# Kernel optimization log

Measured on AMD Instinct MI355X. Metric: run time of the kernel, lower is better.

Reference implementation:

```python
import jax, jax.numpy as jnp
import numpy as np

N_HEADS = 8
NEG_INF = -1e9


def setup_inputs() -> dict:
    key = jax.random.key(0)
    ks = jax.random.split(key, 9)
    B, S, D = 4, 2048, 512
    scale = 1.0 / np.sqrt(D)
    x = jax.random.normal(ks[0], (B, S, D), dtype=jnp.float32)
    mask = jnp.tril(jnp.ones((S, S), dtype=bool))[None, None, :, :]  # causal [1,1,S,S]
    W_Q_w = jax.random.normal(ks[1], (D, D), dtype=jnp.float32) * scale
    W_Q_b = jax.random.normal(ks[2], (D,), dtype=jnp.float32) * 0.02
    W_K_w = jax.random.normal(ks[3], (D, D), dtype=jnp.float32) * scale
    W_K_b = jax.random.normal(ks[4], (D,), dtype=jnp.float32) * 0.02
    W_V_w = jax.random.normal(ks[5], (D, D), dtype=jnp.float32) * scale
    W_V_b = jax.random.normal(ks[6], (D,), dtype=jnp.float32) * 0.02
    W_O_w = jax.random.normal(ks[7], (D, D), dtype=jnp.float32) * scale
    W_O_b = jax.random.normal(ks[8], (D,), dtype=jnp.float32) * 0.02
    return {"x": x, "mask": mask,
            "W_Q_w": W_Q_w, "W_Q_b": W_Q_b, "W_K_w": W_K_w, "W_K_b": W_K_b,
            "W_V_w": W_V_w, "W_V_b": W_V_b, "W_O_w": W_O_w, "W_O_b": W_O_b}


def reference(x, mask, W_Q_w, W_Q_b, W_K_w, W_K_b, W_V_w, W_V_b, W_O_w, W_O_b):
    B, S, D = x.shape
    H = N_HEADS
    Dh = D // H
    # projections (torch Linear: x @ W.T + b), split heads -> [B,H,S,Dh]
    def split_heads(t):
        return t.reshape(B, S, H, Dh).transpose(0, 2, 1, 3)
    Q = split_heads(x @ W_Q_w.T + W_Q_b)
    K = split_heads(x @ W_K_w.T + W_K_b)
    V = split_heads(x @ W_V_w.T + W_V_b)
    # scaled dot-product attention with explicit [B,H,S,S] scores
    scores = jnp.einsum("bhqd,bhkd->bhqk", Q, K) / jnp.sqrt(jnp.float32(Dh))
    scores = jnp.where(mask, scores, jnp.float32(NEG_INF))
    att = jax.nn.softmax(scores, axis=-1)
    out = jnp.einsum("bhqk,bhkd->bhqd", att, V)
    out = out.transpose(0, 2, 1, 3).reshape(B, S, D)
    return out @ W_O_w.T + W_O_b
```

## Files before the change

### kernel.cpp

```cpp
#include <hip/hip_runtime.h>
#include <hip/hip_bf16.h>

#define BATCH 4
#define SEQ   2048
#define DIM   512
#define NH    8
#define DH    64
#define NTOK  (BATCH*SEQ)

typedef __bf16 bf16x8 __attribute__((ext_vector_type(8)));
typedef float  f32x4  __attribute__((ext_vector_type(4)));

#define MFMA16(a,b,c) __builtin_amdgcn_mfma_f32_16x16x32_bf16((a),(b),(c),0,0,0)

#if __has_builtin(__builtin_amdgcn_exp2f)
#define EXP2F(x) __builtin_amdgcn_exp2f(x)
#else
#define EXP2F(x) exp2f(x)
#endif

#define QSCALE 0.18033688011112042f

typedef __attribute__((address_space(1))) void GAS;
typedef __attribute__((address_space(3))) void LAS;
__device__ __forceinline__ void gl_lds16(const void* g, void* l) {
  __builtin_amdgcn_global_load_lds((GAS*)g, (LAS*)l, 16, 0, 0);
}

__global__ __launch_bounds__(256) void cvt_f32_bf16(const float* __restrict__ src,
                                                    __bf16* __restrict__ dst, int n8) {
  int i = blockIdx.x * blockDim.x + threadIdx.x;
  if (i >= n8) return;
  const float4* s = (const float4*)src;
  float4 a = s[2*i], b = s[2*i+1];
  bf16x8 o;
  o[0] = (__bf16)a.x; o[1] = (__bf16)a.y; o[2] = (__bf16)a.z; o[3] = (__bf16)a.w;
  o[4] = (__bf16)b.x; o[5] = (__bf16)b.y; o[6] = (__bf16)b.z; o[7] = (__bf16)b.w;
  *(bf16x8*)&dst[8*i] = o;
}

__global__ __launch_bounds__(256) void cvt_weights(
    const float* __restrict__ s0, const float* __restrict__ s1,
    const float* __restrict__ s2, const float* __restrict__ s3,
    __bf16* __restrict__ o0, __bf16* __restrict__ o1,
    __bf16* __restrict__ o2, __bf16* __restrict__ o3) {
  int i = blockIdx.x * blockDim.x + threadIdx.x;
  const int which = i >> 15, off = i & 32767;
  const float* src = (which == 0) ? s0 : (which == 1) ? s1 : (which == 2) ? s2 : s3;
  __bf16* dst      = (which == 0) ? o0 : (which == 1) ? o1 : (which == 2) ? o2 : o3;
  const float4* s = (const float4*)src;
  float4 a = s[2*off], b = s[2*off+1];
  bf16x8 o;
  o[0] = (__bf16)a.x; o[1] = (__bf16)a.y; o[2] = (__bf16)a.z; o[3] = (__bf16)a.w;
  o[4] = (__bf16)b.x; o[5] = (__bf16)b.y; o[6] = (__bf16)b.z; o[7] = (__bf16)b.w;
  *(bf16x8*)&dst[8*off] = o;
}

__global__ __launch_bounds__(256) void gemm_qkv(
    const __bf16* __restrict__ xb,
    const __bf16* __restrict__ wq, const __bf16* __restrict__ wk,
    const __bf16* __restrict__ wv,
    const float* __restrict__ bq, const float* __restrict__ bk,
    const float* __restrict__ bv,
    __bf16* __restrict__ Qb, __bf16* __restrict__ Kb, __bf16* __restrict__ Vt)
{
  const int z = blockIdx.z;
  const __bf16* W    = (z == 0) ? wq : (z == 1) ? wk : wv;
  const float*  bias = (z == 0) ? bq : (z == 1) ? bk : bv;

  __shared__ __align__(16) __bf16 As[128*64];
  __shared__ __align__(16) __bf16 Bs[128*64];

  const int tid  = threadIdx.x;
  const int m0   = blockIdx.x * 128, n0 = blockIdx.y * 128;
  const int w    = tid >> 6, lane = tid & 63, quad = lane >> 4, l16 = lane & 15;
  const int wm   = (w >> 1) * 64, wn = (w & 1) * 64;
  const int srow = w*32 + (lane >> 3);
  const int scc  = (lane & 7) * 8;

  f32x4 acc[4][4] = {};

  for (int k0 = 0; k0 < DIM; k0 += 64) {
#pragma unroll
    for (int i = 0; i < 4; ++i) {
      const int row = srow + i*8;
      gl_lds16(&xb[(size_t)(m0+row)*DIM + k0 + scc], &As[(w*4+i)*512]);
      gl_lds16(&W [(size_t)(n0+row)*DIM + k0 + scc], &Bs[(w*4+i)*512]);
    }
    __syncthreads();
#pragma unroll
    for (int kk = 0; kk < 2; ++kk) {
      const int ko = kk*32 + quad*8;
      bf16x8 af[4], bfr[4];
#pragma unroll
      for (int f = 0; f < 4; ++f) {
        af[f]  = *(const bf16x8*)&As[(wm + f*16 + l16)*64 + ko];
        bfr[f] = *(const bf16x8*)&Bs[(wn + f*16 + l16)*64 + ko];
      }
#pragma unroll
      for (int fm = 0; fm < 4; ++fm)
#pragma unroll
        for (int fn = 0; fn < 4; ++fn)
          acc[fm][fn] = MFMA16(af[fm], bfr[fn], acc[fm][fn]);
    }
    __syncthreads();
  }

#pragma unroll
  for (int fm = 0; fm < 4; ++fm) {
#pragma unroll
    for (int fn = 0; fn < 4; ++fn) {
      const int col  = n0 + wn + fn*16 + l16;
      const float bc = bias[col];
      const int h = col >> 6, dh = col & 63;
#pragma unroll
      for (int r = 0; r < 4; ++r) {
        const int row = m0 + wm + fm*16 + quad*4 + r;
        const int b = row >> 11, s = row & 2047;
        const float v = acc[fm][fn][r] + bc;
        if (z == 2) {
          Vt[((size_t)(b*NH + h)*DH + dh)*SEQ + s] = (__bf16)v;
        } else if (z == 0) {
          Qb[((size_t)(b*NH + h)*SEQ + s)*DH + dh] = (__bf16)(v * QSCALE);
        } else {
          Kb[((size_t)(b*NH + h)*SEQ + s)*DH + dh] = (__bf16)v;
        }
      }
    }
  }
}

__global__ __launch_bounds__(256) void gemm_out(
    const __bf16* __restrict__ attnb, const __bf16* __restrict__ wo,
    const float* __restrict__ bo, float* __restrict__ out)
{
  __shared__ __align__(16) __bf16 As[128*64];
  __shared__ __align__(16) __bf16 Bs[128*64];

  const int tid = threadIdx.x;
  const int m0  = blockIdx.x * 128, n0 = blockIdx.y * 128;
  const int w   = tid >> 6, lane = tid & 63, quad = lane >> 4, l16 = lane & 15;
  const int wm  = (w >> 1) * 64, wn = (w & 1) * 64;
  const int srow = w*32 + (lane >> 3);
  const int scc  = (lane & 7) * 8;

  f32x4 acc[4][4] = {};

  for (int k0 = 0; k0 < DIM; k0 += 64) {
#pragma unroll
    for (int i = 0; i < 4; ++i) {
      const int row = srow + i*8;
      gl_lds16(&attnb[(size_t)(m0+row)*DIM + k0 + scc], &As[(w*4+i)*512]);
      gl_lds16(&wo   [(size_t)(n0+row)*DIM + k0 + scc], &Bs[(w*4+i)*512]);
    }
    __syncthreads();
#pragma unroll
    for (int kk = 0; kk < 2; ++kk) {
      const int ko = kk*32 + quad*8;
      bf16x8 af[4], bfr[4];
#pragma unroll
      for (int f = 0; f < 4; ++f) {
        af[f]  = *(const bf16x8*)&As[(wm + f*16 + l16)*64 + ko];
        bfr[f] = *(const bf16x8*)&Bs[(wn + f*16 + l16)*64 + ko];
      }
#pragma unroll
      for (int fm = 0; fm < 4; ++fm)
#pragma unroll
        for (int fn = 0; fn < 4; ++fn)
          acc[fm][fn] = MFMA16(af[fm], bfr[fn], acc[fm][fn]);
    }
    __syncthreads();
  }

#pragma unroll
  for (int fm = 0; fm < 4; ++fm) {
#pragma unroll
    for (int fn = 0; fn < 4; ++fn) {
      const int col  = n0 + wn + fn*16 + l16;
      const float bc = bo[col];
#pragma unroll
      for (int r = 0; r < 4; ++r) {
        const int row = m0 + wm + fm*16 + quad*4 + r;
        out[(size_t)row*DIM + col] = acc[fm][fn][r] + bc;
      }
    }
  }
}

__global__ __launch_bounds__(64) void flash_attn(
    const __bf16* __restrict__ Qb, const __bf16* __restrict__ Kb,
    const __bf16* __restrict__ Vt, __bf16* __restrict__ attnb)
{
  const int idx = blockIdx.x;
  const int bh  = idx & 31;
  const int t   = 63 - (idx >> 5);
  const int b   = bh >> 3, h = bh & 7;
  const int lane = threadIdx.x & 63, quad = lane >> 4, l16 = lane & 15;
  const int q0  = t * 32;

  const __bf16* Qp = Qb + (size_t)bh * SEQ * DH;
  const __bf16* Kp = Kb + (size_t)bh * SEQ * DH;
  const __bf16* Vp = Vt + (size_t)bh * DH * SEQ;

  __shared__ __align__(16) __bf16 Pw[32*72];

  bf16x8 qf[2][2];
#pragma unroll
  for (int mf = 0; mf < 2; ++mf)
#pragma unroll
    for (int kk = 0; kk < 2; ++kk)
      qf[mf][kk] = *(const bf16x8*)&Qp[(size_t)(q0 + mf*16 + l16)*DH + kk*32 + quad*8];

  f32x4 of[2][4] = {};
  float m_[2][4], l_[2][4];
#pragma unroll
  for (int mf = 0; mf < 2; ++mf)
#pragma unroll
    for (int r = 0; r < 4; ++r) { m_[mf][r] = -1e30f; l_[mf][r] = 0.f; }

  const int ktiles = (q0 >> 6) + 1;

  bf16x8 kfA[4][2], kfB[4][2];
#pragma unroll
  for (int fn = 0; fn < 4; ++fn)
#pragma unroll
    for (int kk = 0; kk < 2; ++kk)
      kfA[fn][kk] = *(const bf16x8*)&Kp[(size_t)(fn*16 + l16)*DH + kk*32 + quad*8];

#define TILE_STEP(KC, KN, KT)                                                  \
  {                                                                            \
    const int k0 = (KT) * 64;                                                  \
                   \
    bf16x8 vf[4][2];                                                           \
    _Pragma("unroll")                                                          \
    for (int nd = 0; nd < 4; ++nd)                                             \
      _Pragma("unroll")                                                        \
      for (int kq = 0; kq < 2; ++kq)                                           \
        vf[nd][kq] = *(const bf16x8*)&Vp[(size_t)(nd*16 + l16)*SEQ + k0 +      \
                                         kq*32 + quad*8];                      \
                               \
    {                                                                          \
      const int kn0 = ((KT) + 1 < ktiles) ? k0 + 64 : 0;                       \
      _Pragma("unroll")                                                        \
      for (int fn = 0; fn < 4; ++fn)                                           \
        _Pragma("unroll")                                                      \
        for (int kk = 0; kk < 2; ++kk)                                         \
          KN[fn][kk] = *(const bf16x8*)&Kp[(size_t)(kn0 + fn*16 + l16)*DH +    \
                                           kk*32 + quad*8];                    \
    }                                                                          \
                                   \
    f32x4 sf[2][4] = {};                                                       \
    __builtin_amdgcn_s_setprio(1);                                             \
    _Pragma("unroll")                                                          \
    for (int mf = 0; mf < 2; ++mf)                                             \
      _Pragma("unroll")                                                        \
      for (int fn = 0; fn < 4; ++fn) {                                         \
        sf[mf][fn] = MFMA16(qf[mf][0], KC[fn][0], sf[mf][fn]);                 \
        sf[mf][fn] = MFMA16(qf[mf][1], KC[fn][1], sf[mf][fn]);                 \
      }                                                                        \
    __builtin_amdgcn_s_setprio(0);                                             \
                               \
    if (k0 + 63 > q0) {                                                        \
      _Pragma("unroll")                                                        \
      for (int mf = 0; mf < 2; ++mf)                                           \
        _Pragma("unroll")                                                      \
        for (int fn = 0; fn < 4; ++fn) {                                       \
          const int col = k0 + fn*16 + l16;                                    \
          _Pragma("unroll")                                                    \
          for (int r = 0; r < 4; ++r) {                                        \
            const int row = q0 + mf*16 + quad*4 + r;                           \
            if (col > row) sf[mf][fn][r] = -1e30f;                             \
          }                                                                    \
        }                                                                      \
    }                                                                          \
         \
    float rmax[2][4];                                                          \
    _Pragma("unroll")                                                          \
    for (int mf = 0; mf < 2; ++mf)                                             \
      _Pragma("unroll")                                                        \
      for (int r = 0; r < 4; ++r)                                              \
        rmax[mf][r] = fmaxf(fmaxf(sf[mf][0][r], sf[mf][1][r]),                 \
                            fmaxf(sf[mf][2][r], sf[mf][3][r]));                \
    _Pragma("unroll")                                                          \
    for (int d = 1; d < 16; d <<= 1)                                           \
      _Pragma("unroll")                                                        \
      for (int mf = 0; mf < 2; ++mf)                                           \
        _Pragma("unroll")                                                      \
        for (int r = 0; r < 4; ++r)                                            \
          rmax[mf][r] = fmaxf(rmax[mf][r], __shfl_xor(rmax[mf][r], d));        \
                    \
    _Pragma("unroll")                                                          \
    for (int mf = 0; mf < 2; ++mf)                                             \
      _Pragma("unroll")                                                        \
      for (int r = 0; r < 4; ++r) {                                            \
        const float mn = fmaxf(m_[mf][r], rmax[mf][r]);                        \
        const float al = EXP2F(m_[mf][r] - mn);                                \
        m_[mf][r] = mn;                                                        \
        l_[mf][r] *= al;                                                       \
        _Pragma("unroll")                                                      \
        for (int nd = 0; nd < 4; ++nd) of[mf][nd][r] *= al;                    \
      }                                                                        \
    _Pragma("unroll")                                                          \
    for (int mf = 0; mf < 2; ++mf)                                             \
      _Pragma("unroll")                                                        \
      for (int fn = 0; fn < 4; ++fn)                                           \
        _Pragma("unroll")                                                      \
        for (int r = 0; r < 4; ++r)                                            \
          sf[mf][fn][r] = EXP2F(sf[mf][fn][r] - m_[mf][r]);                    \
    _Pragma("unroll")                                                          \
    for (int mf = 0; mf < 2; ++mf)                                             \
      _Pragma("unroll")                                                        \
      for (int r = 0; r < 4; ++r)                                              \
        l_[mf][r] += (sf[mf][0][r] + sf[mf][1][r]) +                           \
                     (sf[mf][2][r] + sf[mf][3][r]);                            \
                                           \
    _Pragma("unroll")                                                          \
    for (int mf = 0; mf < 2; ++mf)                                             \
      _Pragma("unroll")                                                        \
      for (int fn = 0; fn < 4; ++fn)                                           \
        _Pragma("unroll")                                                      \
        for (int r = 0; r < 4; ++r)                                            \
          Pw[(mf*16 + quad*4 + r)*72 + fn*16 + l16] = (__bf16)sf[mf][fn][r];   \
    bf16x8 pa[2][2];                                                           \
    _Pragma("unroll")                                                          \
    for (int mf = 0; mf < 2; ++mf)                                             \
      _Pragma("unroll")                                                        \
      for (int kq = 0; kq < 2; ++kq)                                           \
        pa[mf][kq] = *(const bf16x8*)&Pw[(mf*16 + l16)*72 + kq*32 + quad*8];   \
                                                      \
    __builtin_amdgcn_s_setprio(1);                                             \
    _Pragma("unroll")                                                          \
    for (int mf = 0; mf < 2; ++mf)                                             \
      _Pragma("unroll")                                                        \
      for (int nd = 0; nd < 4; ++nd) {                                         \
        of[mf][nd] = MFMA16(pa[mf][0], vf[nd][0], of[mf][nd]);                 \
        of[mf][nd] = MFMA16(pa[mf][1], vf[nd][1], of[mf][nd]);                 \
      }                                                                        \
    __builtin_amdgcn_s_setprio(0);                                             \
  }

  for (int kt = 0; kt < ktiles; kt += 2) {
    TILE_STEP(kfA, kfB, kt);
    if (kt + 1 < ktiles) TILE_STEP(kfB, kfA, kt + 1);
  }
#undef TILE_STEP

#pragma unroll
  for (int d = 1; d < 16; d <<= 1)
#pragma unroll
    for (int mf = 0; mf < 2; ++mf)
#pragma unroll
      for (int r = 0; r < 4; ++r)
        l_[mf][r] += __shfl_xor(l_[mf][r], d);
#pragma unroll
  for (int mf = 0; mf < 2; ++mf)
#pragma unroll
    for (int r = 0; r < 4; ++r)
      l_[mf][r] = 1.0f / l_[mf][r];
#pragma unroll
  for (int mf = 0; mf < 2; ++mf)
#pragma unroll
    for (int nd = 0; nd < 4; ++nd) {
      const int dh = nd*16 + l16;
#pragma unroll
      for (int r = 0; r < 4; ++r) {
        const int q = q0 + mf*16 + quad*4 + r;
        attnb[((size_t)b*SEQ + q)*DIM + h*DH + dh] = (__bf16)(of[mf][nd][r] * l_[mf][r]);
      }
    }
}

extern "C" void kernel_launch(void* const* d_in, const int* in_sizes, int n_in,
                              void* d_out, int out_size, void* d_ws, size_t ws_size,
                              hipStream_t stream) {
  const float* x  = (const float*)d_in[0];
  const float* Wq = (const float*)d_in[2];
  const float* bq = (const float*)d_in[3];
  const float* Wk = (const float*)d_in[4];
  const float* bk = (const float*)d_in[5];
  const float* Wv = (const float*)d_in[6];
  const float* bv = (const float*)d_in[7];
  const float* Wo = (const float*)d_in[8];
  const float* bo = (const float*)d_in[9];
  float* out = (float*)d_out;

  __bf16* xb    = (__bf16*)d_ws;
  __bf16* wq    = xb + (size_t)NTOK*DIM;
  __bf16* wk    = wq + DIM*DIM;
  __bf16* wv    = wk + DIM*DIM;
  __bf16* wo    = wv + DIM*DIM;
  __bf16* Qb    = wo + DIM*DIM;
  __bf16* Kb    = Qb + (size_t)NTOK*DIM;
  __bf16* Vt    = Kb + (size_t)NTOK*DIM;
  __bf16* attnb = Vt + (size_t)NTOK*DIM;

  cvt_f32_bf16<<<(NTOK*DIM/8)/256, 256, 0, stream>>>(x, xb, NTOK*DIM/8);
  cvt_weights<<<(4*DIM*DIM/8)/256, 256, 0, stream>>>(Wq, Wk, Wv, Wo, wq, wk, wv, wo);

  gemm_qkv<<<dim3(NTOK/128, DIM/128, 3), 256, 0, stream>>>(
      xb, wq, wk, wv, bq, bk, bv, Qb, Kb, Vt);

  flash_attn<<<2048, 64, 0, stream>>>(Qb, Kb, Vt, attnb);

  gemm_out<<<dim3(NTOK/128, DIM/128), 256, 0, stream>>>(attnb, wo, bo, out);
}
```

Measured before the change: 213.7 us.

## Split KV tiles across two waves and pair causal query tiles per block

The flash attention kernel now runs two waves per block. Each wave takes alternating 64-key tiles, and the partial softmax states (max, sum, output) are merged through shared memory before wave 0 writes the result. Each block also handles two query tiles, p and 63-p, in turn, so the causal work per block is roughly equal. The grid shrinks to 1024 blocks. This costs extra shared memory, two block-wide barriers per query tile and a merge step.

```diff
diff --git a/kernel.cpp b/kernel.cpp
--- a/kernel.cpp
+++ b/kernel.cpp
@@ -187,45 +187,51 @@
   }
 }
 
-__global__ __launch_bounds__(64) void flash_attn(
+__global__ __launch_bounds__(128) void flash_attn(
     const __bf16* __restrict__ Qb, const __bf16* __restrict__ Kb,
     const __bf16* __restrict__ Vt, __bf16* __restrict__ attnb)
 {
   const int idx = blockIdx.x;
   const int bh  = idx & 31;
-  const int t   = 63 - (idx >> 5);
+  const int p   = idx >> 5;
   const int b   = bh >> 3, h = bh & 7;
-  const int lane = threadIdx.x & 63, quad = lane >> 4, l16 = lane & 15;
-  const int q0  = t * 32;
+  const int tid = threadIdx.x;
+  const int wv  = tid >> 6;
+  const int lane = tid & 63, quad = lane >> 4, l16 = lane & 15;
 
   const __bf16* Qp = Qb + (size_t)bh * SEQ * DH;
   const __bf16* Kp = Kb + (size_t)bh * SEQ * DH;
   const __bf16* Vp = Vt + (size_t)bh * DH * SEQ;
 
-  __shared__ __align__(16) __bf16 Pw[32*72];
-
-  bf16x8 qf[2][2];
-#pragma unroll
-  for (int mf = 0; mf < 2; ++mf)
-#pragma unroll
-    for (int kk = 0; kk < 2; ++kk)
-      qf[mf][kk] = *(const bf16x8*)&Qp[(size_t)(q0 + mf*16 + l16)*DH + kk*32 + quad*8];
-
-  f32x4 of[2][4] = {};
-  float m_[2][4], l_[2][4];
-#pragma unroll
-  for (int mf = 0; mf < 2; ++mf)
-#pragma unroll
-    for (int r = 0; r < 4; ++r) { m_[mf][r] = -1e30f; l_[mf][r] = 0.f; }
-
-  const int ktiles = (q0 >> 6) + 1;
-
-  bf16x8 kfA[4][2], kfB[4][2];
-#pragma unroll
-  for (int fn = 0; fn < 4; ++fn)
-#pragma unroll
-    for (int kk = 0; kk < 2; ++kk)
-      kfA[fn][kk] = *(const bf16x8*)&Kp[(size_t)(fn*16 + l16)*DH + kk*32 + quad*8];
+  __shared__ __align__(16) __bf16 Pw2[2*32*72];
+  __shared__ __align__(16) float  Mg[64*48];
+  __bf16* Pw = Pw2 + wv*(32*72);
+
+  for (int ph = 0; ph < 2; ++ph) {
+    const int tq = ph ? (63 - p) : p;
+    const int q0 = tq * 32;
+    const int ktiles = (q0 >> 6) + 1;
+
+    bf16x8 qf[2][2];
+#pragma unroll
+    for (int mf = 0; mf < 2; ++mf)
+#pragma unroll
+      for (int kk = 0; kk < 2; ++kk)
+        qf[mf][kk] = *(const bf16x8*)&Qp[(size_t)(q0 + mf*16 + l16)*DH + kk*32 + quad*8];
+
+    f32x4 of[2][4] = {};
+    float m_[2][4], l_[2][4];
+#pragma unroll
+    for (int mf = 0; mf < 2; ++mf)
+#pragma unroll
+      for (int r = 0; r < 4; ++r) { m_[mf][r] = -1e30f; l_[mf][r] = 0.f; }
+
+    bf16x8 kfA[4][2], kfB[4][2];
+#pragma unroll
+    for (int fn = 0; fn < 4; ++fn)
+#pragma unroll
+      for (int kk = 0; kk < 2; ++kk)
+        kfA[fn][kk] = *(const bf16x8*)&Kp[(size_t)(wv*64 + fn*16 + l16)*DH + kk*32 + quad*8];
 
 #define TILE_STEP(KC, KN, KT)                                                  \
   {                                                                            \
@@ -238,9 +244,9 @@
       for (int kq = 0; kq < 2; ++kq)                                           \
         vf[nd][kq] = *(const bf16x8*)&Vp[(size_t)(nd*16 + l16)*SEQ + k0 +      \
                                          kq*32 + quad*8];                      \
-                               \
+        \
     {                                                                          \
-      const int kn0 = ((KT) + 1 < ktiles) ? k0 + 64 : 0;                       \
+      const int kn0 = ((KT) + 2 < ktiles) ? k0 + 128 : 0;                      \
       _Pragma("unroll")                                                        \
       for (int fn = 0; fn < 4; ++fn)                                           \
         _Pragma("unroll")                                                      \
@@ -313,7 +319,7 @@
       for (int r = 0; r < 4; ++r)                                              \
         l_[mf][r] += (sf[mf][0][r] + sf[mf][1][r]) +                           \
                      (sf[mf][2][r] + sf[mf][3][r]);                            \
-                                           \
+                          \
     _Pragma("unroll")                                                          \
     for (int mf = 0; mf < 2; ++mf)                                             \
       _Pragma("unroll")                                                        \
@@ -339,35 +345,66 @@
     __builtin_amdgcn_s_setprio(0);                                             \
   }
 
-  for (int kt = 0; kt < ktiles; kt += 2) {
-    TILE_STEP(kfA, kfB, kt);
-    if (kt + 1 < ktiles) TILE_STEP(kfB, kfA, kt + 1);
-  }
+    for (int kt = wv; kt < ktiles; kt += 4) {
+      TILE_STEP(kfA, kfB, kt);
+      if (kt + 2 < ktiles) TILE_STEP(kfB, kfA, kt + 2);
+    }
 #undef TILE_STEP
 
-#pragma unroll
-  for (int d = 1; d < 16; d <<= 1)
-#pragma unroll
-    for (int mf = 0; mf < 2; ++mf)
-#pragma unroll
-      for (int r = 0; r < 4; ++r)
-        l_[mf][r] += __shfl_xor(l_[mf][r], d);
-#pragma unroll
-  for (int mf = 0; mf < 2; ++mf)
-#pragma unroll
-    for (int r = 0; r < 4; ++r)
-      l_[mf][r] = 1.0f / l_[mf][r];
-#pragma unroll
-  for (int mf = 0; mf < 2; ++mf)
-#pragma unroll
-    for (int nd = 0; nd < 4; ++nd) {
-      const int dh = nd*16 + l16;
-#pragma unroll
-      for (int r = 0; r < 4; ++r) {
-        const int q = q0 + mf*16 + quad*4 + r;
-        attnb[((size_t)b*SEQ + q)*DIM + h*DH + dh] = (__bf16)(of[mf][nd][r] * l_[mf][r]);
-      }
-    }
+    if (wv == 1) {
+      float* C = Mg + lane*48;
+#pragma unroll
+      for (int mf = 0; mf < 2; ++mf)
+#pragma unroll
+        for (int r = 0; r < 4; ++r) { C[mf*4+r] = m_[mf][r]; C[8+mf*4+r] = l_[mf][r]; }
+#pragma unroll
+      for (int mf = 0; mf < 2; ++mf)
+#pragma unroll
+        for (int nd = 0; nd < 4; ++nd)
+          *(f32x4*)&C[16 + (mf*4+nd)*4] = of[mf][nd];
+    }
+    __syncthreads();
+    if (wv == 0) {
+      const float* C = Mg + lane*48;
+#pragma unroll
+      for (int mf = 0; mf < 2; ++mf)
+#pragma unroll
+        for (int r = 0; r < 4; ++r) {
+          const float mo = C[mf*4+r], lo = C[8+mf*4+r];
+          const float mn = fmaxf(m_[mf][r], mo);
+          const float a  = EXP2F(m_[mf][r] - mn);
+          const float bt = EXP2F(mo - mn);
+          l_[mf][r] = l_[mf][r]*a + lo*bt;
+#pragma unroll
+          for (int nd = 0; nd < 4; ++nd)
+            of[mf][nd][r] = of[mf][nd][r]*a + C[16 + (mf*4+nd)*4 + r]*bt;
+        }
+#pragma unroll
+      for (int d = 1; d < 16; d <<= 1)
+#pragma unroll
+        for (int mf = 0; mf < 2; ++mf)
+#pragma unroll
+          for (int r = 0; r < 4; ++r)
+            l_[mf][r] += __shfl_xor(l_[mf][r], d);
+#pragma unroll
+      for (int mf = 0; mf < 2; ++mf)
+#pragma unroll
+        for (int r = 0; r < 4; ++r)
+          l_[mf][r] = 1.0f / l_[mf][r];
+#pragma unroll
+      for (int mf = 0; mf < 2; ++mf)
+#pragma unroll
+        for (int nd = 0; nd < 4; ++nd) {
+          const int dh = nd*16 + l16;
+#pragma unroll
+          for (int r = 0; r < 4; ++r) {
+            const int q = q0 + mf*16 + quad*4 + r;
+            attnb[((size_t)b*SEQ + q)*DIM + h*DH + dh] = (__bf16)(of[mf][nd][r] * l_[mf][r]);
+          }
+        }
+    }
+    __syncthreads();
+  }
 }
 
 extern "C" void kernel_launch(void* const* d_in, const int* in_sizes, int n_in,
@@ -400,7 +437,7 @@
   gemm_qkv<<<dim3(NTOK/128, DIM/128, 3), 256, 0, stream>>>(
       xb, wq, wk, wv, bq, bk, bv, Qb, Kb, Vt);
 
-  flash_attn<<<2048, 64, 0, stream>>>(Qb, Kb, Vt, attnb);
+  flash_attn<<<1024, 128, 0, stream>>>(Qb, Kb, Vt, attnb);
 
   gemm_out<<<dim3(NTOK/128, DIM/128), 256, 0, stream>>>(attnb, wo, bo, out);
 }
```

After: 224.3 us. +5.0%, slower.
